# Optimization experiments

Hardware: AMD Instinct MI355X
Metric: run time of the kernel (lower is better)

## Reference

```python
import jax, jax.numpy as jnp
import numpy as np

B, N, DIM = 8, 8192, 512
H, DH = 8, 64
HID = H * DH  # 512
TCD = 512
EPS_LN = 1e-5
EPS_NORM = 1e-12


def layer_norm(x, gamma):
    m = jnp.mean(x, axis=-1, keepdims=True)
    v = jnp.var(x, axis=-1, keepdims=True)
    return (x - m) / jnp.sqrt(v + EPS_LN) * gamma


def rms_head_norm(t, gamma):
    # t: [b,h,n,d], gamma: [h,1,d]; F.normalize(dim=-1) * sqrt(d) * gamma
    nrm = jnp.sqrt(jnp.sum(t * t, axis=-1, keepdims=True))
    return t / jnp.maximum(nrm, EPS_NORM) * (DH ** 0.5) * gamma


def setup_inputs() -> dict:
    key = jax.random.key(0)
    ks = jax.random.split(key, 8)
    return {
        "x": jax.random.normal(ks[0], (B, N, DIM), dtype=jnp.float32),
        "time": jax.random.normal(ks[1], (B, TCD), dtype=jnp.float32),
        "ln_gamma": jnp.ones((DIM,), dtype=jnp.float32),
        "w_time": jax.random.normal(ks[2], (TCD, 2 * DIM), dtype=jnp.float32) * 0.02,
        "b_time": jnp.zeros((2 * DIM,), dtype=jnp.float32),
        "w_qkv": jax.random.normal(ks[3], (DIM, 3 * HID), dtype=jnp.float32) * (1.0 / DIM ** 0.5),
        "g_q": jnp.ones((H, 1, DH), dtype=jnp.float32),
        "g_k": jnp.ones((H, 1, DH), dtype=jnp.float32),
        "w_out": jax.random.normal(ks[4], (HID, DIM), dtype=jnp.float32) * (1.0 / HID ** 0.5),
        "ln_out_gamma": jnp.ones((DIM,), dtype=jnp.float32),
    }


def reference(x, time, ln_gamma, w_time, b_time, w_qkv, g_q, g_k, w_out, ln_out_gamma):
    scale = DH ** -0.5
    x = layer_norm(x, ln_gamma)
    # time conditioning: SiLU -> Linear -> [b,1,2*dim] -> chunk
    t = jax.nn.silu(time) @ w_time + b_time          # [b, 2*dim]
    t = t[:, None, :]                                 # [b, 1, 2*dim]
    t_scale, t_shift = jnp.split(t, 2, axis=-1)
    x = x * (t_scale + 1.0) + t_shift
    # qkv projection and head split
    qkv = x @ w_qkv                                   # [b, n, 3*hid]
    q, k, v = jnp.split(qkv, 3, axis=-1)
    to_heads = lambda t: t.reshape(B, N, H, DH).transpose(0, 2, 1, 3)  # [b,h,n,d]
    q, k, v = to_heads(q), to_heads(k), to_heads(v)
    q = rms_head_norm(q, g_q)
    k = rms_head_norm(k, g_k)
    q = jax.nn.softmax(q, axis=-1) * scale            # softmax over d
    k = jax.nn.softmax(k, axis=-2)                    # softmax over n
    context = jnp.einsum('bhnd,bhne->bhde', k, v)     # [b,h,d,e]
    out = jnp.einsum('bhde,bhnd->bhne', context, q)   # [b,h,n,e]
    out = out.transpose(0, 2, 1, 3).reshape(B, N, HID)
    out = out @ w_out
    return layer_norm(out, ln_out_gamma)
```

## Files before the change

kernel.cpp:

```cpp
#include <hip/hip_runtime.h>
#include <cstdint>
#include <cmath>

#define BB   8
#define NN   8192
#define DIMC 512
#define HH   8
#define DHD  64
#define HIDC 512
#define TCDC 512

typedef __attribute__((ext_vector_type(8))) short bf16x8;
typedef __attribute__((ext_vector_type(4))) float f32x4;

__device__ inline void split2(float v, short* hi, short* lo) {
  unsigned u = __float_as_uint(v);
  float hf = __uint_as_float(u & 0xFFFF0000u);
  *hi = (short)(u >> 16);
  *lo = (short)(__float_as_uint(v - hf) >> 16);
}

__device__ inline void gload16(const void* g, void* l) {
  __builtin_amdgcn_global_load_lds(
      (const __attribute__((address_space(1))) unsigned*)g,
      (__attribute__((address_space(3))) unsigned*)l, 16, 0, 0);
}

__global__ __launch_bounds__(256) void k_prep_w(
    const float* __restrict__ w, short* __restrict__ whi, short* __restrict__ wlo) {
  int nblk = blockIdx.x, ktile = blockIdx.y;
  int tid = threadIdx.x;
  size_t obase = ((size_t)(nblk * 16 + ktile)) * 4096;
  for (int i = tid; i < 4096; i += 256) {
    int kl = i >> 7, col = i & 127;
    float v = w[(size_t)(ktile * 32 + kl) * 1536 + nblk * 128 + col];
    short h, l; split2(v, &h, &l);
    size_t o = obase + ((size_t)((kl >> 3) * 128 + col)) * 8 + (kl & 7);
    whi[o] = h; wlo[o] = l;
  }
}

__global__ __launch_bounds__(256) void k_time_mlp(
    const float* __restrict__ timev, const float* __restrict__ w_time,
    const float* __restrict__ b_time, const float* __restrict__ ln_gamma,
    float* __restrict__ cs, float* __restrict__ ct) {
  int b = blockIdx.x;
  int d = blockIdx.y * 256 + threadIdx.x;
  int tid = threadIdx.x;
  __shared__ float st[TCDC];
  for (int k = tid; k < TCDC; k += 256) {
    float v = timev[b * TCDC + k];
    st[k] = v / (1.f + __expf(-v));
  }
  __syncthreads();
  float accs = b_time[d];
  float acct = b_time[DIMC + d];
  for (int k = 0; k < TCDC; ++k) {
    float s = st[k];
    accs = fmaf(s, w_time[k * (2 * DIMC) + d], accs);
    acct = fmaf(s, w_time[k * (2 * DIMC) + DIMC + d], acct);
  }
  cs[b * DIMC + d] = ln_gamma[d] * (1.f + accs);
  ct[b * DIMC + d] = acct;
}

__global__ __launch_bounds__(256) void k_rowstats(
    const float* __restrict__ x, float* __restrict__ mean, float* __restrict__ rstd) {
  int row = blockIdx.x * 4 + (threadIdx.x >> 6);
  int lane = threadIdx.x & 63;
  const float4* xr = (const float4*)(x + (size_t)row * DIMC);
  float s = 0.f, s2 = 0.f;
#pragma unroll
  for (int i = 0; i < 2; ++i) {
    float4 v = xr[lane + 64 * i];
    s  += v.x + v.y + v.z + v.w;
    s2 += v.x * v.x + v.y * v.y + v.z * v.z + v.w * v.w;
  }
#pragma unroll
  for (int m = 1; m < 64; m <<= 1) { s += __shfl_xor(s, m); s2 += __shfl_xor(s2, m); }
  float mu = s * (1.f / DIMC);
  float var = s2 * (1.f / DIMC) - mu * mu;
  if (lane == 0) { mean[row] = mu; rstd[row] = rsqrtf(var + 1e-5f); }
}

__global__ __launch_bounds__(256) void k_qkv_gemm(
    const float* __restrict__ x,
    const short* __restrict__ whi, const short* __restrict__ wlo,
    const float* __restrict__ mean, const float* __restrict__ rstd,
    const float* __restrict__ cs, const float* __restrict__ ct,
    const float* __restrict__ g_q, const float* __restrict__ g_k,
    short* __restrict__ qhi, short* __restrict__ qlo,
    float* __restrict__ k_n, float* __restrict__ v_h) {
  __shared__ __align__(16) short As[2][4][128][8];
  __shared__ __align__(16) short Bs[2][4][128][8];
  int tid = threadIdx.x;
  int lane = tid & 63, wave = tid >> 6;
  int wr = wave >> 1, wc = wave & 1;
  int l15 = lane & 15, g = lane >> 4;
  int nblk = blockIdx.x, n0 = nblk * 128;
  int m0 = blockIdx.y * 128;
  int b = m0 >> 13;

  f32x4 acc[4][4];
#pragma unroll
  for (int mi = 0; mi < 4; ++mi)
#pragma unroll
    for (int ni = 0; ni < 4; ++ni) acc[mi][ni] = (f32x4){0.f, 0.f, 0.f, 0.f};

  int arow = tid >> 2;
  int akc  = tid & 3;
  float mu0 = mean[m0 + arow],      rs0 = rstd[m0 + arow];
  float mu1 = mean[m0 + arow + 64], rs1 = rstd[m0 + arow + 64];

  for (int kt = 0; kt < 16; ++kt) {
    const float4 c1a = *(const float4*)(cs + b * DIMC + kt * 32 + akc * 8);
    const float4 c1b = *(const float4*)(cs + b * DIMC + kt * 32 + akc * 8 + 4);
    const float4 c2a = *(const float4*)(ct + b * DIMC + kt * 32 + akc * 8);
    const float4 c2b = *(const float4*)(ct + b * DIMC + kt * 32 + akc * 8 + 4);
#pragma unroll
    for (int half = 0; half < 2; ++half) {
      int row = arow + half * 64;
      float mu = half ? mu1 : mu0, rs = half ? rs1 : rs0;
      const float4* xa = (const float4*)(x + (size_t)(m0 + row) * DIMC + kt * 32 + akc * 8);
      float4 a0 = xa[0], a1 = xa[1];
      float vv[8];
      vv[0] = fmaf((a0.x - mu) * rs, c1a.x, c2a.x);
      vv[1] = fmaf((a0.y - mu) * rs, c1a.y, c2a.y);
      vv[2] = fmaf((a0.z - mu) * rs, c1a.z, c2a.z);
      vv[3] = fmaf((a0.w - mu) * rs, c1a.w, c2a.w);
      vv[4] = fmaf((a1.x - mu) * rs, c1b.x, c2b.x);
      vv[5] = fmaf((a1.y - mu) * rs, c1b.y, c2b.y);
      vv[6] = fmaf((a1.z - mu) * rs, c1b.z, c2b.z);
      vv[7] = fmaf((a1.w - mu) * rs, c1b.w, c2b.w);
      bf16x8 vh, vl;
#pragma unroll
      for (int i = 0; i < 8; ++i) {
        short hh, ll; split2(vv[i], &hh, &ll);
        vh[i] = hh; vl[i] = ll;
      }
      *(bf16x8*)&As[0][akc][row ^ akc][0] = vh;
      *(bf16x8*)&As[1][akc][row ^ akc][0] = vl;
    }
    size_t boff = ((size_t)(nblk * 16 + kt)) * 4096;
#pragma unroll
    for (int h = 0; h < 2; ++h) {
      const short* src = (h ? wlo : whi) + boff;
      short* dst = &Bs[h][0][0][0];
#pragma unroll
      for (int r = 0; r < 2; ++r) {
        int ci = (r * 4 + wave) * 64 + lane;
        gload16(src + (size_t)ci * 8, dst + (r * 4 + wave) * 512);
      }
    }
    __syncthreads();
    bf16x8 ah[4], al[4], bh[4], bl[4];
#pragma unroll
    for (int i = 0; i < 4; ++i) {
      int row = wr * 64 + i * 16 + l15;
      ah[i] = *(const bf16x8*)&As[0][g][row ^ g][0];
      al[i] = *(const bf16x8*)&As[1][g][row ^ g][0];
      int col = wc * 64 + i * 16 + l15;
      bh[i] = *(const bf16x8*)&Bs[0][g][col][0];
      bl[i] = *(const bf16x8*)&Bs[1][g][col][0];
    }
#pragma unroll
    for (int mi = 0; mi < 4; ++mi)
#pragma unroll
      for (int ni = 0; ni < 4; ++ni) {
        acc[mi][ni] = __builtin_amdgcn_mfma_f32_16x16x32_bf16(ah[mi], bh[ni], acc[mi][ni], 0, 0, 0);
        acc[mi][ni] = __builtin_amdgcn_mfma_f32_16x16x32_bf16(ah[mi], bl[ni], acc[mi][ni], 0, 0, 0);
        acc[mi][ni] = __builtin_amdgcn_mfma_f32_16x16x32_bf16(al[mi], bh[ni], acc[mi][ni], 0, 0, 0);
      }
    __syncthreads();
  }

  int section = n0 >> 9;
  int h = ((n0 & 511) >> 6) + wc;
  float gq[4], gk[4];
  int kt_[4], kb_[4], kk_[4];
#pragma unroll
  for (int ni = 0; ni < 4; ++ni) {
    int ch = ni * 16 + l15;
    int hid = h * 64 + ch;
    gq[ni] = g_q[hid]; gk[ni] = g_k[hid];
    kt_[ni] = hid >> 5; kb_[ni] = (hid >> 3) & 3; kk_[ni] = hid & 7;
  }
#pragma unroll
  for (int mi = 0; mi < 4; ++mi) {
#pragma unroll
    for (int rg = 0; rg < 4; ++rg) {
      int grow = m0 + wr * 64 + mi * 16 + g * 4 + rg;
      float v[4];
#pragma unroll
      for (int ni = 0; ni < 4; ++ni) v[ni] = acc[mi][ni][rg];
      if (section == 2) {
        int nrow = grow & (NN - 1);
#pragma unroll
        for (int ni = 0; ni < 4; ++ni)
          v_h[((size_t)(b * HH + h) * NN + nrow) * DHD + ni * 16 + l15] = v[ni];
      } else {
        float ss = v[0] * v[0] + v[1] * v[1] + v[2] * v[2] + v[3] * v[3];
#pragma unroll
        for (int mk = 1; mk < 16; mk <<= 1) ss += __shfl_xor(ss, mk);
        float sc = 8.f / fmaxf(sqrtf(ss), 1e-12f);
        if (section == 0) {
#pragma unroll
          for (int ni = 0; ni < 4; ++ni) v[ni] *= sc * gq[ni];
          float mx = fmaxf(fmaxf(v[0], v[1]), fmaxf(v[2], v[3]));
#pragma unroll
          for (int mk = 1; mk < 16; mk <<= 1) mx = fmaxf(mx, __shfl_xor(mx, mk));
#pragma unroll
          for (int ni = 0; ni < 4; ++ni) v[ni] = __expf(v[ni] - mx);
          float se = v[0] + v[1] + v[2] + v[3];
#pragma unroll
          for (int mk = 1; mk < 16; mk <<= 1) se += __shfl_xor(se, mk);
          float inv = 0.125f / se;
          int mblk = grow >> 7, r = grow & 127;
#pragma unroll
          for (int ni = 0; ni < 4; ++ni) {
            short hh, ll; split2(v[ni] * inv, &hh, &ll);
            size_t o = (((size_t)(mblk * 16 + kt_[ni]) * 4 + kb_[ni]) * 128 + r) * 8 + kk_[ni];
            qhi[o] = hh; qlo[o] = ll;
          }
        } else {
          int nrow = grow & (NN - 1);
#pragma unroll
          for (int ni = 0; ni < 4; ++ni)
            k_n[((size_t)(b * HH + h) * NN + nrow) * DHD + ni * 16 + l15] = v[ni] * sc * gk[ni];
        }
      }
    }
  }
}

__global__ __launch_bounds__(256) void k_kmax_part(
    const float* __restrict__ k_n, float* __restrict__ kmp) {
  int bh = blockIdx.x, chunk = blockIdx.y;
  int d = threadIdx.x & 63, ng = threadIdx.x >> 6;
  const float* base = k_n + ((size_t)bh * NN + chunk * 1024) * DHD;
  float m = -1e30f;
  for (int n = ng; n < 1024; n += 4) m = fmaxf(m, base[(size_t)n * DHD + d]);
  __shared__ float red[256];
  red[threadIdx.x] = m;
  __syncthreads();
  if (threadIdx.x < 64) {
    m = fmaxf(fmaxf(red[d], red[64 + d]), fmaxf(red[128 + d], red[192 + d]));
    kmp[(bh * 8 + chunk) * DHD + d] = m;
  }
}

__global__ __launch_bounds__(256) void k_kmax_red(
    const float* __restrict__ kmp, float* __restrict__ km) {
  int i = blockIdx.x * 256 + threadIdx.x;
  int bh = i >> 6, d = i & 63;
  float m = -1e30f;
  for (int c = 0; c < 8; ++c) m = fmaxf(m, kmp[(bh * 8 + c) * DHD + d]);
  km[i] = m;
}

__global__ __launch_bounds__(256) void k_ctx_part(
    const float* __restrict__ k_n, const float* __restrict__ v_h,
    const float* __restrict__ km, float* __restrict__ Cp, float* __restrict__ Zp) {
  int bh = blockIdx.x, chunk = blockIdx.y;
  int d = threadIdx.x & 63, eg = threadIdx.x >> 6;
  size_t base = ((size_t)bh * NN + chunk * 1024) * DHD;
  float kmd = km[bh * DHD + d];
  float acc[16];
#pragma unroll
  for (int j = 0; j < 16; ++j) acc[j] = 0.f;
  float z = 0.f;
  for (int n = 0; n < 1024; ++n) {
    float ek = __expf(k_n[base + (size_t)n * DHD + d] - kmd);
    z += ek;
    const float4* vr = (const float4*)(v_h + base + (size_t)n * DHD + eg * 16);
    float4 q0 = vr[0], q1 = vr[1], q2 = vr[2], q3 = vr[3];
    acc[0] = fmaf(ek, q0.x, acc[0]);   acc[1] = fmaf(ek, q0.y, acc[1]);
    acc[2] = fmaf(ek, q0.z, acc[2]);   acc[3] = fmaf(ek, q0.w, acc[3]);
    acc[4] = fmaf(ek, q1.x, acc[4]);   acc[5] = fmaf(ek, q1.y, acc[5]);
    acc[6] = fmaf(ek, q1.z, acc[6]);   acc[7] = fmaf(ek, q1.w, acc[7]);
    acc[8] = fmaf(ek, q2.x, acc[8]);   acc[9] = fmaf(ek, q2.y, acc[9]);
    acc[10] = fmaf(ek, q2.z, acc[10]); acc[11] = fmaf(ek, q2.w, acc[11]);
    acc[12] = fmaf(ek, q3.x, acc[12]); acc[13] = fmaf(ek, q3.y, acc[13]);
    acc[14] = fmaf(ek, q3.z, acc[14]); acc[15] = fmaf(ek, q3.w, acc[15]);
  }
  size_t co = ((size_t)(bh * 8 + chunk) * DHD + d) * DHD + eg * 16;
  float4* cp4 = (float4*)(Cp + co);
  cp4[0] = make_float4(acc[0], acc[1], acc[2], acc[3]);
  cp4[1] = make_float4(acc[4], acc[5], acc[6], acc[7]);
  cp4[2] = make_float4(acc[8], acc[9], acc[10], acc[11]);
  cp4[3] = make_float4(acc[12], acc[13], acc[14], acc[15]);
  if (eg == 0) Zp[(bh * 8 + chunk) * DHD + d] = z;
}

__global__ __launch_bounds__(256) void k_ctx_red(
    const float* __restrict__ Cp, const float* __restrict__ Zp, float* __restrict__ Cn) {
  int bh = blockIdx.x;
  int tid = threadIdx.x;
  __shared__ float zs[64];
  if (tid < 64) {
    float zt = 0.f;
    for (int c = 0; c < 8; ++c) zt += Zp[(bh * 8 + c) * DHD + tid];
    zs[tid] = 1.f / zt;
  }
  __syncthreads();
  for (int i = tid; i < DHD * DHD; i += 256) {
    int d = i >> 6;
    float s = 0.f;
    for (int c = 0; c < 8; ++c) s += Cp[(size_t)(bh * 8 + c) * (DHD * DHD) + i];
    Cn[(size_t)bh * (DHD * DHD) + i] = s * zs[d];
  }
}

__global__ __launch_bounds__(256) void k_mstack(
    const float* __restrict__ Cn, const float* __restrict__ w_out,
    short* __restrict__ mhi, short* __restrict__ mlo) {
  int bh = blockIdx.x;
  int b = bh >> 3, h = bh & 7;
  int j0 = blockIdx.y * 256;
  int tid = threadIdx.x;
  int d = tid & 63, jg = tid >> 6;
  __shared__ float Cs[64][65];
  for (int i = tid; i < 4096; i += 256) Cs[i >> 6][i & 63] = Cn[(size_t)bh * 4096 + i];
  __syncthreads();
  int ktile = h * 2 + (d >> 5), kblk = (d >> 3) & 3, kk = d & 7;
  for (int jj = 0; jj < 64; ++jj) {
    int j = j0 + jg * 64 + jj;
    float s = 0.f;
#pragma unroll 16
    for (int e = 0; e < 64; ++e) s = fmaf(Cs[d][e], w_out[(size_t)(h * 64 + e) * DIMC + j], s);
    short hh, ll; split2(s, &hh, &ll);
    size_t o = ((((size_t)(b * 4 + (j >> 7)) * 16 + ktile) * 4 + kblk) * 128 + (j & 127)) * 8 + kk;
    mhi[o] = hh; mlo[o] = ll;
  }
}

__global__ __launch_bounds__(256) void k_out_gemm(
    const short* __restrict__ qhi, const short* __restrict__ qlo,
    const short* __restrict__ mhi, const short* __restrict__ mlo,
    float* __restrict__ out) {
  __shared__ __align__(16) short As[2][4][128][8];
  __shared__ __align__(16) short Bs[2][4][128][8];
  int tid = threadIdx.x;
  int lane = tid & 63, wave = tid >> 6;
  int wr = wave >> 1, wc = wave & 1;
  int l15 = lane & 15, g = lane >> 4;
  int nblk = blockIdx.x, n0 = nblk * 128;
  int mblk = blockIdx.y, m0 = mblk * 128;
  int b = m0 >> 13;

  f32x4 acc[4][4];
#pragma unroll
  for (int mi = 0; mi < 4; ++mi)
#pragma unroll
    for (int ni = 0; ni < 4; ++ni) acc[mi][ni] = (f32x4){0.f, 0.f, 0.f, 0.f};

  for (int kt = 0; kt < 16; ++kt) {
    size_t aoff = ((size_t)(mblk * 16 + kt)) * 4096;
    size_t boff = ((size_t)((b * 4 + nblk) * 16 + kt)) * 4096;
#pragma unroll
    for (int h = 0; h < 2; ++h) {
      const short* asrc = (h ? qlo : qhi) + aoff;
      const short* bsrc = (h ? mlo : mhi) + boff;
#pragma unroll
      for (int r = 0; r < 2; ++r) {
        int ci = (r * 4 + wave) * 64 + lane;
        gload16(asrc + (size_t)ci * 8, &As[h][0][0][0] + (r * 4 + wave) * 512);
        gload16(bsrc + (size_t)ci * 8, &Bs[h][0][0][0] + (r * 4 + wave) * 512);
      }
    }
    __syncthreads();
    bf16x8 ah[4], al[4], bh[4], bl[4];
#pragma unroll
    for (int i = 0; i < 4; ++i) {
      int row = wr * 64 + i * 16 + l15;
      ah[i] = *(const bf16x8*)&As[0][g][row][0];
      al[i] = *(const bf16x8*)&As[1][g][row][0];
      int col = wc * 64 + i * 16 + l15;
      bh[i] = *(const bf16x8*)&Bs[0][g][col][0];
      bl[i] = *(const bf16x8*)&Bs[1][g][col][0];
    }
#pragma unroll
    for (int mi = 0; mi < 4; ++mi)
#pragma unroll
      for (int ni = 0; ni < 4; ++ni) {
        acc[mi][ni] = __builtin_amdgcn_mfma_f32_16x16x32_bf16(ah[mi], bh[ni], acc[mi][ni], 0, 0, 0);
        acc[mi][ni] = __builtin_amdgcn_mfma_f32_16x16x32_bf16(ah[mi], bl[ni], acc[mi][ni], 0, 0, 0);
        acc[mi][ni] = __builtin_amdgcn_mfma_f32_16x16x32_bf16(al[mi], bh[ni], acc[mi][ni], 0, 0, 0);
      }
    __syncthreads();
  }
#pragma unroll
  for (int mi = 0; mi < 4; ++mi)
#pragma unroll
    for (int rg = 0; rg < 4; ++rg) {
      int grow = m0 + wr * 64 + mi * 16 + g * 4 + rg;
#pragma unroll
      for (int ni = 0; ni < 4; ++ni)
        out[(size_t)grow * DIMC + n0 + wc * 64 + ni * 16 + l15] = acc[mi][ni][rg];
    }
}

__global__ __launch_bounds__(256) void k_ln_out(
    float* __restrict__ y, const float* __restrict__ gamma) {
  int row = blockIdx.x * 4 + (threadIdx.x >> 6);
  int lane = threadIdx.x & 63;
  float4* yr = (float4*)(y + (size_t)row * DIMC);
  float4 v0 = yr[lane], v1 = yr[lane + 64];
  float s = v0.x + v0.y + v0.z + v0.w + v1.x + v1.y + v1.z + v1.w;
  float s2 = v0.x * v0.x + v0.y * v0.y + v0.z * v0.z + v0.w * v0.w +
             v1.x * v1.x + v1.y * v1.y + v1.z * v1.z + v1.w * v1.w;
#pragma unroll
  for (int m = 1; m < 64; m <<= 1) { s += __shfl_xor(s, m); s2 += __shfl_xor(s2, m); }
  float mu = s * (1.f / DIMC);
  float rs = rsqrtf(s2 * (1.f / DIMC) - mu * mu + 1e-5f);
  const float4* gp = (const float4*)gamma;
  float4 g0 = gp[lane], g1 = gp[lane + 64];
  v0.x = (v0.x - mu) * rs * g0.x; v0.y = (v0.y - mu) * rs * g0.y;
  v0.z = (v0.z - mu) * rs * g0.z; v0.w = (v0.w - mu) * rs * g0.w;
  v1.x = (v1.x - mu) * rs * g1.x; v1.y = (v1.y - mu) * rs * g1.y;
  v1.z = (v1.z - mu) * rs * g1.z; v1.w = (v1.w - mu) * rs * g1.w;
  yr[lane] = v0; yr[lane + 64] = v1;
}

extern "C" void kernel_launch(void* const* d_in, const int* in_sizes, int n_in,
                              void* d_out, int out_size, void* d_ws, size_t ws_size,
                              hipStream_t stream) {
  (void)in_sizes; (void)n_in; (void)out_size; (void)ws_size;
  const float* x        = (const float*)d_in[0];
  const float* timev    = (const float*)d_in[1];
  const float* ln_gamma = (const float*)d_in[2];
  const float* w_time   = (const float*)d_in[3];
  const float* b_time   = (const float*)d_in[4];
  const float* w_qkv    = (const float*)d_in[5];
  const float* g_q      = (const float*)d_in[6];
  const float* g_k      = (const float*)d_in[7];
  const float* w_out    = (const float*)d_in[8];
  const float* ln_out_g = (const float*)d_in[9];
  float* out = (float*)d_out;

  float* cs   = (float*)d_ws;
  float* ct   = cs + 4096;
  float* mean = ct + 4096;
  float* rstd = mean + 65536;
  float* kmp  = rstd + 65536;
  float* km   = kmp + 32768;
  float* Zp   = km + 4096;
  float* Cp   = Zp + 32768;
  float* Cn   = Cp + 2097152;
  float* k_n  = Cn + 262144;
  short* whi  = (short*)(k_n + 33554432);
  short* wlo  = whi + 786432;
  short* qhi  = wlo + 786432;
  short* qlo  = qhi + 33554432;
  short* mhi  = (short*)Cp;
  short* mlo  = mhi + 2097152;
  float* v_h  = out;

  hipLaunchKernelGGL(k_prep_w, dim3(12, 16), dim3(256), 0, stream, w_qkv, whi, wlo);
  hipLaunchKernelGGL(k_time_mlp, dim3(BB, 2), dim3(256), 0, stream,
                     timev, w_time, b_time, ln_gamma, cs, ct);
  hipLaunchKernelGGL(k_rowstats, dim3(BB * NN / 4), dim3(256), 0, stream, x, mean, rstd);
  hipLaunchKernelGGL(k_qkv_gemm, dim3(12, 512), dim3(256), 0, stream,
                     x, whi, wlo, mean, rstd, cs, ct, g_q, g_k, qhi, qlo, k_n, v_h);
  hipLaunchKernelGGL(k_kmax_part, dim3(64, 8), dim3(256), 0, stream, k_n, kmp);
  hipLaunchKernelGGL(k_kmax_red, dim3(16), dim3(256), 0, stream, kmp, km);
  hipLaunchKernelGGL(k_ctx_part, dim3(64, 8), dim3(256), 0, stream, k_n, v_h, km, Cp, Zp);
  hipLaunchKernelGGL(k_ctx_red, dim3(64), dim3(256), 0, stream, Cp, Zp, Cn);
  hipLaunchKernelGGL(k_mstack, dim3(64, 2), dim3(256), 0, stream, Cn, w_out, mhi, mlo);
  hipLaunchKernelGGL(k_out_gemm, dim3(4, 512), dim3(256), 0, stream, qhi, qlo, mhi, mlo, out);
  hipLaunchKernelGGL(k_ln_out, dim3(BB * NN / 4), dim3(256), 0, stream, out, ln_out_g);
}
```

Measured before the change: 1.396 ms.

## Fuse key exp and normalizer into QKV epilogue and compute context with MFMA

The key softmax over n no longer subtracts a per-column maximum. The QKV GEMM epilogue now computes exp of the normalized keys directly, stores exp(k) and v as hi/lo bf16 tiles, and accumulates the column sums with atomics. This removes the separate kmax kernels and the k_n round trip. The scalar FMA context kernel is replaced by a split-bf16 MFMA GEMM, and both large GEMMs get a tile-order swizzle for better cache locality. Dropping the max subtraction relies on the RMS-normalized keys staying bounded (about 8·|g_k|), so a large g_k could overflow the exp.

Result: faster. 1.232 ms (-11.8%).

```diff
diff --git a/kernel.cpp b/kernel.cpp
--- a/kernel.cpp
+++ b/kernel.cpp
@@ -83,6 +83,10 @@
   if (lane == 0) { mean[row] = mu; rstd[row] = rsqrtf(var + 1e-5f); }
 }
 
+__global__ __launch_bounds__(256) void k_zero(float* __restrict__ Zg) {
+  Zg[blockIdx.x * 256 + threadIdx.x] = 0.f;
+}
+
 __global__ __launch_bounds__(256) void k_qkv_gemm(
     const float* __restrict__ x,
     const short* __restrict__ whi, const short* __restrict__ wlo,
@@ -90,15 +94,20 @@
     const float* __restrict__ cs, const float* __restrict__ ct,
     const float* __restrict__ g_q, const float* __restrict__ g_k,
     short* __restrict__ qhi, short* __restrict__ qlo,
-    float* __restrict__ k_n, float* __restrict__ v_h) {
+    short* __restrict__ ekhi, short* __restrict__ eklo,
+    short* __restrict__ vhi, short* __restrict__ vlo,
+    float* __restrict__ Zg) {
   __shared__ __align__(16) short As[2][4][128][8];
   __shared__ __align__(16) short Bs[2][4][128][8];
   int tid = threadIdx.x;
   int lane = tid & 63, wave = tid >> 6;
   int wr = wave >> 1, wc = wave & 1;
   int l15 = lane & 15, g = lane >> 4;
-  int nblk = blockIdx.x, n0 = nblk * 128;
-  int m0 = blockIdx.y * 128;
+  int o = blockIdx.y * 12 + blockIdx.x;
+  int tile = (o & 7) * 768 + (o >> 3);
+  int mblk = tile / 12, nblk = tile - mblk * 12;
+  int n0 = nblk * 128;
+  int m0 = mblk * 128;
   int b = m0 >> 13;
 
   f32x4 acc[4][4];
@@ -176,138 +185,174 @@
 
   int section = n0 >> 9;
   int h = ((n0 & 511) >> 6) + wc;
-  float gq[4], gk[4];
-  int kt_[4], kb_[4], kk_[4];
-#pragma unroll
-  for (int ni = 0; ni < 4; ++ni) {
-    int ch = ni * 16 + l15;
-    int hid = h * 64 + ch;
-    gq[ni] = g_q[hid]; gk[ni] = g_k[hid];
-    kt_[ni] = hid >> 5; kb_[ni] = (hid >> 3) & 3; kk_[ni] = hid & 7;
-  }
-#pragma unroll
-  for (int mi = 0; mi < 4; ++mi) {
-#pragma unroll
-    for (int rg = 0; rg < 4; ++rg) {
-      int grow = m0 + wr * 64 + mi * 16 + g * 4 + rg;
-      float v[4];
-#pragma unroll
-      for (int ni = 0; ni < 4; ++ni) v[ni] = acc[mi][ni][rg];
-      if (section == 2) {
+  int bh = b * HH + h;
+  if (section == 2) {
+#pragma unroll
+    for (int mi = 0; mi < 4; ++mi)
+#pragma unroll
+      for (int rg = 0; rg < 4; ++rg) {
+        int grow = m0 + wr * 64 + mi * 16 + g * 4 + rg;
         int nrow = grow & (NN - 1);
-#pragma unroll
-        for (int ni = 0; ni < 4; ++ni)
-          v_h[((size_t)(b * HH + h) * NN + nrow) * DHD + ni * 16 + l15] = v[ni];
-      } else {
+        size_t tb = (((size_t)(bh * 8 + (nrow >> 10)) * 32 + ((nrow >> 5) & 31)) * 4 +
+                     ((nrow >> 3) & 3)) * 512 + (nrow & 7);
+#pragma unroll
+        for (int ni = 0; ni < 4; ++ni) {
+          short hh, ll; split2(acc[mi][ni][rg], &hh, &ll);
+          size_t oo = tb + (size_t)(ni * 16 + l15) * 8;
+          vhi[oo] = hh; vlo[oo] = ll;
+        }
+      }
+  } else if (section == 0) {
+    float gq[4];
+    int kt_[4], kb_[4], kk_[4];
+#pragma unroll
+    for (int ni = 0; ni < 4; ++ni) {
+      int hid = h * 64 + ni * 16 + l15;
+      gq[ni] = g_q[hid];
+      kt_[ni] = hid >> 5; kb_[ni] = (hid >> 3) & 3; kk_[ni] = hid & 7;
+    }
+#pragma unroll
+    for (int mi = 0; mi < 4; ++mi)
+#pragma unroll
+      for (int rg = 0; rg < 4; ++rg) {
+        int grow = m0 + wr * 64 + mi * 16 + g * 4 + rg;
+        float v[4];
+#pragma unroll
+        for (int ni = 0; ni < 4; ++ni) v[ni] = acc[mi][ni][rg];
         float ss = v[0] * v[0] + v[1] * v[1] + v[2] * v[2] + v[3] * v[3];
 #pragma unroll
         for (int mk = 1; mk < 16; mk <<= 1) ss += __shfl_xor(ss, mk);
         float sc = 8.f / fmaxf(sqrtf(ss), 1e-12f);
-        if (section == 0) {
-#pragma unroll
-          for (int ni = 0; ni < 4; ++ni) v[ni] *= sc * gq[ni];
-          float mx = fmaxf(fmaxf(v[0], v[1]), fmaxf(v[2], v[3]));
-#pragma unroll
-          for (int mk = 1; mk < 16; mk <<= 1) mx = fmaxf(mx, __shfl_xor(mx, mk));
-#pragma unroll
-          for (int ni = 0; ni < 4; ++ni) v[ni] = __expf(v[ni] - mx);
-          float se = v[0] + v[1] + v[2] + v[3];
-#pragma unroll
-          for (int mk = 1; mk < 16; mk <<= 1) se += __shfl_xor(se, mk);
-          float inv = 0.125f / se;
-          int mblk = grow >> 7, r = grow & 127;
-#pragma unroll
-          for (int ni = 0; ni < 4; ++ni) {
-            short hh, ll; split2(v[ni] * inv, &hh, &ll);
-            size_t o = (((size_t)(mblk * 16 + kt_[ni]) * 4 + kb_[ni]) * 128 + r) * 8 + kk_[ni];
-            qhi[o] = hh; qlo[o] = ll;
-          }
-        } else {
-          int nrow = grow & (NN - 1);
-#pragma unroll
-          for (int ni = 0; ni < 4; ++ni)
-            k_n[((size_t)(b * HH + h) * NN + nrow) * DHD + ni * 16 + l15] = v[ni] * sc * gk[ni];
+#pragma unroll
+        for (int ni = 0; ni < 4; ++ni) v[ni] *= sc * gq[ni];
+        float mx = fmaxf(fmaxf(v[0], v[1]), fmaxf(v[2], v[3]));
+#pragma unroll
+        for (int mk = 1; mk < 16; mk <<= 1) mx = fmaxf(mx, __shfl_xor(mx, mk));
+#pragma unroll
+        for (int ni = 0; ni < 4; ++ni) v[ni] = __expf(v[ni] - mx);
+        float se = v[0] + v[1] + v[2] + v[3];
+#pragma unroll
+        for (int mk = 1; mk < 16; mk <<= 1) se += __shfl_xor(se, mk);
+        float inv = 0.125f / se;
+        int mblk2 = grow >> 7, r = grow & 127;
+#pragma unroll
+        for (int ni = 0; ni < 4; ++ni) {
+          short hh, ll; split2(v[ni] * inv, &hh, &ll);
+          size_t oo = (((size_t)(mblk2 * 16 + kt_[ni]) * 4 + kb_[ni]) * 128 + r) * 8 + kk_[ni];
+          qhi[oo] = hh; qlo[oo] = ll;
         }
       }
-    }
-  }
-}
-
-__global__ __launch_bounds__(256) void k_kmax_part(
-    const float* __restrict__ k_n, float* __restrict__ kmp) {
-  int bh = blockIdx.x, chunk = blockIdx.y;
-  int d = threadIdx.x & 63, ng = threadIdx.x >> 6;
-  const float* base = k_n + ((size_t)bh * NN + chunk * 1024) * DHD;
-  float m = -1e30f;
-  for (int n = ng; n < 1024; n += 4) m = fmaxf(m, base[(size_t)n * DHD + d]);
-  __shared__ float red[256];
-  red[threadIdx.x] = m;
-  __syncthreads();
-  if (threadIdx.x < 64) {
-    m = fmaxf(fmaxf(red[d], red[64 + d]), fmaxf(red[128 + d], red[192 + d]));
-    kmp[(bh * 8 + chunk) * DHD + d] = m;
-  }
-}
-
-__global__ __launch_bounds__(256) void k_kmax_red(
-    const float* __restrict__ kmp, float* __restrict__ km) {
-  int i = blockIdx.x * 256 + threadIdx.x;
-  int bh = i >> 6, d = i & 63;
-  float m = -1e30f;
-  for (int c = 0; c < 8; ++c) m = fmaxf(m, kmp[(bh * 8 + c) * DHD + d]);
-  km[i] = m;
-}
-
-__global__ __launch_bounds__(256) void k_ctx_part(
-    const float* __restrict__ k_n, const float* __restrict__ v_h,
-    const float* __restrict__ km, float* __restrict__ Cp, float* __restrict__ Zp) {
-  int bh = blockIdx.x, chunk = blockIdx.y;
-  int d = threadIdx.x & 63, eg = threadIdx.x >> 6;
-  size_t base = ((size_t)bh * NN + chunk * 1024) * DHD;
-  float kmd = km[bh * DHD + d];
-  float acc[16];
-#pragma unroll
-  for (int j = 0; j < 16; ++j) acc[j] = 0.f;
-  float z = 0.f;
-  for (int n = 0; n < 1024; ++n) {
-    float ek = __expf(k_n[base + (size_t)n * DHD + d] - kmd);
-    z += ek;
-    const float4* vr = (const float4*)(v_h + base + (size_t)n * DHD + eg * 16);
-    float4 q0 = vr[0], q1 = vr[1], q2 = vr[2], q3 = vr[3];
-    acc[0] = fmaf(ek, q0.x, acc[0]);   acc[1] = fmaf(ek, q0.y, acc[1]);
-    acc[2] = fmaf(ek, q0.z, acc[2]);   acc[3] = fmaf(ek, q0.w, acc[3]);
-    acc[4] = fmaf(ek, q1.x, acc[4]);   acc[5] = fmaf(ek, q1.y, acc[5]);
-    acc[6] = fmaf(ek, q1.z, acc[6]);   acc[7] = fmaf(ek, q1.w, acc[7]);
-    acc[8] = fmaf(ek, q2.x, acc[8]);   acc[9] = fmaf(ek, q2.y, acc[9]);
-    acc[10] = fmaf(ek, q2.z, acc[10]); acc[11] = fmaf(ek, q2.w, acc[11]);
-    acc[12] = fmaf(ek, q3.x, acc[12]); acc[13] = fmaf(ek, q3.y, acc[13]);
-    acc[14] = fmaf(ek, q3.z, acc[14]); acc[15] = fmaf(ek, q3.w, acc[15]);
-  }
-  size_t co = ((size_t)(bh * 8 + chunk) * DHD + d) * DHD + eg * 16;
-  float4* cp4 = (float4*)(Cp + co);
-  cp4[0] = make_float4(acc[0], acc[1], acc[2], acc[3]);
-  cp4[1] = make_float4(acc[4], acc[5], acc[6], acc[7]);
-  cp4[2] = make_float4(acc[8], acc[9], acc[10], acc[11]);
-  cp4[3] = make_float4(acc[12], acc[13], acc[14], acc[15]);
-  if (eg == 0) Zp[(bh * 8 + chunk) * DHD + d] = z;
+  } else {
+    float gk[4];
+#pragma unroll
+    for (int ni = 0; ni < 4; ++ni) gk[ni] = g_k[h * 64 + ni * 16 + l15];
+    float zp[4] = {0.f, 0.f, 0.f, 0.f};
+#pragma unroll
+    for (int mi = 0; mi < 4; ++mi)
+#pragma unroll
+      for (int rg = 0; rg < 4; ++rg) {
+        int grow = m0 + wr * 64 + mi * 16 + g * 4 + rg;
+        int nrow = grow & (NN - 1);
+        float v[4];
+#pragma unroll
+        for (int ni = 0; ni < 4; ++ni) v[ni] = acc[mi][ni][rg];
+        float ss = v[0] * v[0] + v[1] * v[1] + v[2] * v[2] + v[3] * v[3];
+#pragma unroll
+        for (int mk = 1; mk < 16; mk <<= 1) ss += __shfl_xor(ss, mk);
+        float sc = 8.f / fmaxf(sqrtf(ss), 1e-12f);
+        size_t tb = (((size_t)(bh * 8 + (nrow >> 10)) * 32 + ((nrow >> 5) & 31)) * 4 +
+                     ((nrow >> 3) & 3)) * 512 + (nrow & 7);
+#pragma unroll
+        for (int ni = 0; ni < 4; ++ni) {
+          float ekv = __expf(v[ni] * sc * gk[ni]);
+          zp[ni] += ekv;
+          short hh, ll; split2(ekv, &hh, &ll);
+          size_t oo = tb + (size_t)(ni * 16 + l15) * 8;
+          ekhi[oo] = hh; eklo[oo] = ll;
+        }
+      }
+#pragma unroll
+    for (int ni = 0; ni < 4; ++ni) {
+      zp[ni] += __shfl_xor(zp[ni], 16);
+      zp[ni] += __shfl_xor(zp[ni], 32);
+    }
+    if (g == 0) {
+#pragma unroll
+      for (int ni = 0; ni < 4; ++ni)
+        atomicAdd(&Zg[bh * 64 + ni * 16 + l15], zp[ni]);
+    }
+  }
+}
+
+__global__ __launch_bounds__(256) void k_ctx(
+    const short* __restrict__ ekhi, const short* __restrict__ eklo,
+    const short* __restrict__ vhi, const short* __restrict__ vlo,
+    float* __restrict__ Cp) {
+  __shared__ __align__(16) short As[2][4][64][8];
+  __shared__ __align__(16) short Bs[2][4][64][8];
+  int tid = threadIdx.x;
+  int lane = tid & 63, wave = tid >> 6;
+  int wr = wave >> 1, wc = wave & 1;
+  int l15 = lane & 15, g = lane >> 4;
+  int bh = blockIdx.x, kc = blockIdx.y;
+  f32x4 acc[2][2];
+#pragma unroll
+  for (int mi = 0; mi < 2; ++mi)
+#pragma unroll
+    for (int nj = 0; nj < 2; ++nj) acc[mi][nj] = (f32x4){0.f, 0.f, 0.f, 0.f};
+
+  size_t cbase = ((size_t)(bh * 8 + kc)) * 32 * 2048;
+  int ci = wave * 64 + lane;
+  for (int kt = 0; kt < 32; ++kt) {
+    size_t tb = cbase + (size_t)kt * 2048 + (size_t)ci * 8;
+    gload16(ekhi + tb, &As[0][0][0][0] + wave * 512);
+    gload16(eklo + tb, &As[1][0][0][0] + wave * 512);
+    gload16(vhi + tb, &Bs[0][0][0][0] + wave * 512);
+    gload16(vlo + tb, &Bs[1][0][0][0] + wave * 512);
+    __syncthreads();
+    bf16x8 ah[2], al[2], bh_[2], bl_[2];
+#pragma unroll
+    for (int i = 0; i < 2; ++i) {
+      int row = wr * 32 + i * 16 + l15;
+      ah[i] = *(const bf16x8*)&As[0][g][row][0];
+      al[i] = *(const bf16x8*)&As[1][g][row][0];
+      int col = wc * 32 + i * 16 + l15;
+      bh_[i] = *(const bf16x8*)&Bs[0][g][col][0];
+      bl_[i] = *(const bf16x8*)&Bs[1][g][col][0];
+    }
+#pragma unroll
+    for (int mi = 0; mi < 2; ++mi)
+#pragma unroll
+      for (int nj = 0; nj < 2; ++nj) {
+        acc[mi][nj] = __builtin_amdgcn_mfma_f32_16x16x32_bf16(ah[mi], bh_[nj], acc[mi][nj], 0, 0, 0);
+        acc[mi][nj] = __builtin_amdgcn_mfma_f32_16x16x32_bf16(ah[mi], bl_[nj], acc[mi][nj], 0, 0, 0);
+        acc[mi][nj] = __builtin_amdgcn_mfma_f32_16x16x32_bf16(al[mi], bh_[nj], acc[mi][nj], 0, 0, 0);
+      }
+    __syncthreads();
+  }
+  float* cp = Cp + ((size_t)(bh * 8 + kc)) * 4096;
+#pragma unroll
+  for (int mi = 0; mi < 2; ++mi)
+#pragma unroll
+    for (int rg = 0; rg < 4; ++rg) {
+      int d = wr * 32 + mi * 16 + g * 4 + rg;
+#pragma unroll
+      for (int nj = 0; nj < 2; ++nj)
+        cp[d * 64 + wc * 32 + nj * 16 + l15] = acc[mi][nj][rg];
+    }
 }
 
 __global__ __launch_bounds__(256) void k_ctx_red(
-    const float* __restrict__ Cp, const float* __restrict__ Zp, float* __restrict__ Cn) {
+    const float* __restrict__ Cp, const float* __restrict__ Zg, float* __restrict__ Cn) {
   int bh = blockIdx.x;
   int tid = threadIdx.x;
   __shared__ float zs[64];
-  if (tid < 64) {
-    float zt = 0.f;
-    for (int c = 0; c < 8; ++c) zt += Zp[(bh * 8 + c) * DHD + tid];
-    zs[tid] = 1.f / zt;
-  }
+  if (tid < 64) zs[tid] = 1.f / Zg[bh * 64 + tid];
   __syncthreads();
   for (int i = tid; i < DHD * DHD; i += 256) {
-    int d = i >> 6;
     float s = 0.f;
-    for (int c = 0; c < 8; ++c) s += Cp[(size_t)(bh * 8 + c) * (DHD * DHD) + i];
-    Cn[(size_t)bh * (DHD * DHD) + i] = s * zs[d];
+    for (int c = 0; c < 8; ++c) s += Cp[(size_t)(bh * 8 + c) * 4096 + i];
+    Cn[(size_t)bh * 4096 + i] = s * zs[i >> 6];
   }
 }
 
@@ -344,8 +389,10 @@
   int lane = tid & 63, wave = tid >> 6;
   int wr = wave >> 1, wc = wave & 1;
   int l15 = lane & 15, g = lane >> 4;
-  int nblk = blockIdx.x, n0 = nblk * 128;
-  int mblk = blockIdx.y, m0 = mblk * 128;
+  int o = blockIdx.y * 4 + blockIdx.x;
+  int tile = (o & 7) * 256 + (o >> 3);
+  int mblk = tile >> 2, nblk = tile & 3;
+  int n0 = nblk * 128, m0 = mblk * 128;
   int b = m0 >> 13;
 
   f32x4 acc[4][4];
@@ -442,30 +489,30 @@
   float* ct   = cs + 4096;
   float* mean = ct + 4096;
   float* rstd = mean + 65536;
-  float* kmp  = rstd + 65536;
-  float* km   = kmp + 32768;
-  float* Zp   = km + 4096;
-  float* Cp   = Zp + 32768;
+  float* Zg   = rstd + 65536;
+  float* Cp   = Zg + 4096;
   float* Cn   = Cp + 2097152;
-  float* k_n  = Cn + 262144;
-  short* whi  = (short*)(k_n + 33554432);
+  short* whi  = (short*)(Cn + 262144);
   short* wlo  = whi + 786432;
   short* qhi  = wlo + 786432;
   short* qlo  = qhi + 33554432;
-  short* mhi  = (short*)Cp;
-  short* mlo  = mhi + 2097152;
-  float* v_h  = out;
+  short* ekhi = qlo + 33554432;
+  short* eklo = ekhi + 33554432;
+  short* mhi  = ekhi;
+  short* mlo  = ekhi + 2097152;
+  short* vhi  = (short*)d_out;
+  short* vlo  = vhi + 33554432;
 
   hipLaunchKernelGGL(k_prep_w, dim3(12, 16), dim3(256), 0, stream, w_qkv, whi, wlo);
   hipLaunchKernelGGL(k_time_mlp, dim3(BB, 2), dim3(256), 0, stream,
                      timev, w_time, b_time, ln_gamma, cs, ct);
   hipLaunchKernelGGL(k_rowstats, dim3(BB * NN / 4), dim3(256), 0, stream, x, mean, rstd);
+  hipLaunchKernelGGL(k_zero, dim3(16), dim3(256), 0, stream, Zg);
   hipLaunchKernelGGL(k_qkv_gemm, dim3(12, 512), dim3(256), 0, stream,
-                     x, whi, wlo, mean, rstd, cs, ct, g_q, g_k, qhi, qlo, k_n, v_h);
-  hipLaunchKernelGGL(k_kmax_part, dim3(64, 8), dim3(256), 0, stream, k_n, kmp);
-  hipLaunchKernelGGL(k_kmax_red, dim3(16), dim3(256), 0, stream, kmp, km);
-  hipLaunchKernelGGL(k_ctx_part, dim3(64, 8), dim3(256), 0, stream, k_n, v_h, km, Cp, Zp);
-  hipLaunchKernelGGL(k_ctx_red, dim3(64), dim3(256), 0, stream, Cp, Zp, Cn);
+                     x, whi, wlo, mean, rstd, cs, ct, g_q, g_k,
+                     qhi, qlo, ekhi, eklo, vhi, vlo, Zg);
+  hipLaunchKernelGGL(k_ctx, dim3(64, 8), dim3(256), 0, stream, ekhi, eklo, vhi, vlo, Cp);
+  hipLaunchKernelGGL(k_ctx_red, dim3(64), dim3(256), 0, stream, Cp, Zg, Cn);
   hipLaunchKernelGGL(k_mstack, dim3(64, 2), dim3(256), 0, stream, Cn, w_out, mhi, mlo);
   hipLaunchKernelGGL(k_out_gemm, dim3(4, 512), dim3(256), 0, stream, qhi, qlo, mhi, mlo, out);
   hipLaunchKernelGGL(k_ln_out, dim3(BB * NN / 4), dim3(256), 0, stream, out, ln_out_g);
```
